# Optimization experiments

Measured on AMD Instinct MI355X. Metric: run time of the kernel, lower is better.

Reference implementation:

```python
import jax, jax.numpy as jnp
import numpy as np

L = 3          # num_layer
E_DIM = 64     # emb_dim
B = 4          # graphs per batch
N = 20000      # nodes per graph
E = 320000     # edges per graph
IN_DIM = 21    # raw node feature dim (Linear(21, emb_dim))
BN_EPS = 1e-5


def setup_inputs() -> dict:
    key = jax.random.key(0)
    ks = jax.random.split(key, 16)
    h2 = 2 * E_DIM
    inp = {
        "x": jax.random.normal(ks[0], (B, N, IN_DIM), dtype=jnp.float32),
        "edge_index": jax.random.randint(ks[1], (B, 2, E), 0, N, dtype=jnp.int64),
        "edge_attr": jax.random.normal(ks[2], (B, E, 1), dtype=jnp.float32),
        # layer-0 input node embedding Linear(21, emb)
        "inW": jax.random.normal(ks[3], (IN_DIM, E_DIM), dtype=jnp.float32) * 0.1,
        "inb": jnp.zeros((E_DIM,), dtype=jnp.float32),
        # per-layer edge encoder Linear(1, emb)
        "edgeW": jax.random.normal(ks[4], (L, 1, E_DIM), dtype=jnp.float32) * 0.1,
        "edgeb": jnp.zeros((L, E_DIM), dtype=jnp.float32),
        # per-layer MLP: Linear(2e,2e) -> BN(2e) -> ReLU -> Linear(2e,e)
        "W1": jax.random.normal(ks[5], (L, h2, h2), dtype=jnp.float32) * 0.05,
        "b1": jnp.zeros((L, h2), dtype=jnp.float32),
        "gamma": jnp.ones((L, h2), dtype=jnp.float32),
        "beta": jnp.zeros((L, h2), dtype=jnp.float32),
        "W2": jax.random.normal(ks[6], (L, h2, E_DIM), dtype=jnp.float32) * 0.05,
        "b2": jnp.zeros((L, E_DIM), dtype=jnp.float32),
    }
    return inp


def _batchnorm_train(h, g, b):
    # BatchNorm1d in training mode: per-graph stats over the node dim, biased var
    m = h.mean(axis=0)
    v = jnp.mean((h - m) ** 2, axis=0)
    return (h - m) * jax.lax.rsqrt(v + BN_EPS) * g + b


def _gin_layer(xg, eig, eag, W1l, b1l, gl, bel, W2l, b2l):
    # xg [N,e], eig [2,E], eag [E,e]
    x_j = xg[eig[0]]                                   # gather source nodes [E,e]
    msg = jnp.concatenate([x_j, eag], axis=-1)         # [E,2e]
    aggr = jax.ops.segment_sum(msg, eig[1], num_segments=N)  # scatter-add [N,2e]
    h = aggr @ W1l + b1l
    h = _batchnorm_train(h, gl, bel)
    h = jax.nn.relu(h)
    return h @ W2l + b2l                               # [N,e]


def reference(x, edge_index, edge_attr, inW, inb, edgeW, edgeb, W1, b1, gamma, beta, W2, b2):
    h = x
    for l in range(L):
        ea = edge_attr @ edgeW[l] + edgeb[l]           # [B,E,e] edge embeddings
        if l == 0:
            h = h @ inW + inb                          # [B,N,e]
        h = jax.vmap(_gin_layer, in_axes=(0, 0, 0, None, None, None, None, None, None))(
            h, edge_index, ea, W1[l], b1[l], gamma[l], beta[l], W2[l], b2[l])
        if l < L - 1:                                  # drop_ratio=0 -> dropout is identity
            h = jax.nn.relu(h)
    return h  # JK='last'
```

## Files before the change

### kernel.cpp

```cpp
#include <hip/hip_runtime.h>
#include <hip/hip_bf16.h>
#include <hip/hip_fp16.h>

#define NB 4
#define NN 20000
#define NE 320000
#define IND 21
#define ED 64
#define H2 128
#define CAP 48
#define NRANGE 32
#define RNODES 625
#define BINCAP 160
#define SCAP 11264
#define BN_EPS 1e-5f

typedef __attribute__((ext_vector_type(8))) short bf16x8;
typedef __attribute__((ext_vector_type(4))) float f32x4;

__device__ __forceinline__ short f2bf(float f) {
    unsigned u = __float_as_uint(f);
    u += 0x7fffu + ((u >> 16) & 1u);
    return (short)(u >> 16);
}

__device__ __forceinline__ void add8(float* ac, const uint4 rv) {
    const float2 f0 = __half22float2(*(const __half2*)&rv.x);
    const float2 f1 = __half22float2(*(const __half2*)&rv.y);
    const float2 f2 = __half22float2(*(const __half2*)&rv.z);
    const float2 f3 = __half22float2(*(const __half2*)&rv.w);
    ac[0] += f0.x; ac[1] += f0.y; ac[2] += f1.x; ac[3] += f1.y;
    ac[4] += f2.x; ac[5] += f2.y; ac[6] += f3.x; ac[7] += f3.y;
}


__global__ __launch_bounds__(256) void k_compact(
    const int* __restrict__ ei, const float* __restrict__ eattr,
    uint2* __restrict__ stage, int* __restrict__ rcnt)
{
    __shared__ uint2 bins[NRANGE][BINCAP];
    __shared__ int lcnt[NRANGE];
    __shared__ int lbase[NRANGE];
    const int b = blockIdx.y;
    const int e0 = blockIdx.x * 2048;
    const int tid = threadIdx.x;
    if (tid < NRANGE) lcnt[tid] = 0;
    __syncthreads();
    const int* srcp = ei + (size_t)b * 2 * NE;
    const int* dstp = srcp + NE;
    const float* ap = eattr + (size_t)b * NE;
    #pragma unroll
    for (int it = 0; it < 8; ++it) {
        const int e = e0 + it * 256 + tid;
        if (e < NE) {
            const int dst = dstp[e];
            const int src = srcp[e];
            const float a = ap[e];
            const int r = dst / RNODES;
            const unsigned lo = ((unsigned)src & 0xffffu) | (__float_as_uint(a) & 0xffff0000u);
            const int p = atomicAdd(&lcnt[r], 1);
            if (p < BINCAP) bins[r][p] = make_uint2(lo, (unsigned)dst);
        }
    }
    __syncthreads();
    if (tid < NRANGE) lbase[tid] = atomicAdd(&rcnt[b * NRANGE + tid], min(lcnt[tid], BINCAP));
    __syncthreads();
    for (int r = 0; r < NRANGE; ++r) {
        const int c = min(lcnt[r], BINCAP);
        uint2* dstg = stage + (size_t)(b * NRANGE + r) * SCAP + lbase[r];
        for (int i = tid; i < c; i += 256) dstg[i] = bins[r][i];
    }
}

__global__ __launch_bounds__(256) void k_scatter(
    const uint2* __restrict__ stage, const int* __restrict__ rcnt,
    int* __restrict__ cnt, unsigned int* __restrict__ bucket)
{
    const int b = blockIdx.x >> 5;
    const int g = blockIdx.x & 31;
    const int count = min(rcnt[b * NRANGE + g], SCAP);
    const uint2* st = stage + (size_t)(b * NRANGE + g) * SCAP;
    for (int idx = threadIdx.x; idx < count; idx += 256) {
        const uint2 rec = st[idx];
        const int node = b * NN + (int)rec.y;
        const int p = atomicAdd(&cnt[node], 1);
        if (p < CAP) bucket[(size_t)node * CAP + p] = rec.x;
    }
}

__global__ __launch_bounds__(256) void k_in(
    const float* __restrict__ x, const float* __restrict__ inW,
    const float* __restrict__ inb, __half* __restrict__ h)
{
    const int b = blockIdx.y;
    const int t = blockIdx.x * 256 + threadIdx.x;
    const int n = t >> 6;
    const int c = t & 63;
    if (n >= NN) return;
    const float* xr = x + ((size_t)b * NN + n) * IND;
    float acc = inb[c];
    #pragma unroll
    for (int k = 0; k < IND; ++k) acc += xr[k] * inW[k * ED + c];
    h[((size_t)b * NN + n) * ED + c] = __float2half(acc);
}

__global__ __launch_bounds__(256) void k_prep(
    const float* __restrict__ W1, const float* __restrict__ W2,
    const float* __restrict__ edgeW, const float* __restrict__ edgeb,
    short* __restrict__ W1T, short* __restrict__ W2T,
    float* __restrict__ uv_all, float* __restrict__ stats_all)
{
    const int l = blockIdx.x;
    const int tid = threadIdx.x;
    ((float4*)(stats_all + l * 1024))[tid] = make_float4(0.f, 0.f, 0.f, 0.f);
    for (int i = tid; i < H2 * ED; i += 256) {
        const int j = i >> 6, k = i & 63;
        W1T[l * 8192 + i] = f2bf(W1[(size_t)l * H2 * H2 + k * H2 + j]);
    }
    for (int i = tid; i < ED * H2; i += 256) {
        const int c = i >> 7, k = i & 127;
        W2T[l * 8192 + i] = f2bf(W2[(size_t)l * H2 * ED + k * ED + c]);
    }
    if (tid < H2) {
        float u = 0.f, v = 0.f;
        for (int k = 0; k < ED; ++k) {
            const float w = W1[(size_t)l * H2 * H2 + (ED + k) * H2 + tid];
            u += edgeW[l * ED + k] * w;
            v += edgeb[l * ED + k] * w;
        }
        uv_all[l * 256 + tid] = u;
        uv_all[l * 256 + H2 + tid] = v;
    }
}


__global__ __launch_bounds__(256, 4) void k_aggr_stats(
    const __half* __restrict__ h, const unsigned int* __restrict__ bucket,
    const int* __restrict__ cnt_arr, const short* __restrict__ W1Tl,
    const float* __restrict__ b1l, const float* __restrict__ uv_l,
    short* __restrict__ aggr_bf, float* __restrict__ s_attr,
    float* __restrict__ stats_l, int write_sattr)
{
    __shared__ short atb[32 * 72];
    __shared__ float sdl[32], ddl[32];
    __shared__ float uL[H2], vL[H2], bbL[H2];
    const int tid = threadIdx.x;
    const int g = blockIdx.x & 7;
    const int b = g >> 1;
    const int t = ((int)blockIdx.x >> 3) * 2 + (g & 1);
    if (t >= NN / 32) return;
    const int n0 = t * 32;

    if (tid < H2) { uL[tid] = uv_l[tid]; vL[tid] = uv_l[H2 + tid]; bbL[tid] = b1l[tid]; }

    {
        const int node = n0 + (tid >> 3);
        const int q = tid & 7;
        const int cntraw = cnt_arr[b * NN + node];
        const int cnt = min(cntraw, CAP);
        const unsigned int* row = bucket + (size_t)(b * NN + node) * CAP;
        const __half* hp = h + (size_t)b * NN * ED + q * 8;
        float ac[8];
        #pragma unroll
        for (int i = 0; i < 8; ++i) ac[i] = 0.f;
        float sa = 0.f;
        int j = 0;
        for (; j + 8 <= cnt; j += 8) {
            const uint4 sA = *(const uint4*)(row + j);
            const uint4 sB = *(const uint4*)(row + j + 4);
            const uint4 r0 = *(const uint4*)(hp + (size_t)(sA.x & 0xffffu) * ED);
            const uint4 r1 = *(const uint4*)(hp + (size_t)(sA.y & 0xffffu) * ED);
            const uint4 r2 = *(const uint4*)(hp + (size_t)(sA.z & 0xffffu) * ED);
            const uint4 r3 = *(const uint4*)(hp + (size_t)(sA.w & 0xffffu) * ED);
            const uint4 r4 = *(const uint4*)(hp + (size_t)(sB.x & 0xffffu) * ED);
            const uint4 r5 = *(const uint4*)(hp + (size_t)(sB.y & 0xffffu) * ED);
            const uint4 r6 = *(const uint4*)(hp + (size_t)(sB.z & 0xffffu) * ED);
            const uint4 r7 = *(const uint4*)(hp + (size_t)(sB.w & 0xffffu) * ED);
            sa += __uint_as_float(sA.x & 0xffff0000u) + __uint_as_float(sA.y & 0xffff0000u)
                + __uint_as_float(sA.z & 0xffff0000u) + __uint_as_float(sA.w & 0xffff0000u)
                + __uint_as_float(sB.x & 0xffff0000u) + __uint_as_float(sB.y & 0xffff0000u)
                + __uint_as_float(sB.z & 0xffff0000u) + __uint_as_float(sB.w & 0xffff0000u);
            add8(ac, r0); add8(ac, r1); add8(ac, r2); add8(ac, r3);
            add8(ac, r4); add8(ac, r5); add8(ac, r6); add8(ac, r7);
        }
        for (; j + 4 <= cnt; j += 4) {
            const uint4 ss = *(const uint4*)(row + j);
            const uint4 r0 = *(const uint4*)(hp + (size_t)(ss.x & 0xffffu) * ED);
            const uint4 r1 = *(const uint4*)(hp + (size_t)(ss.y & 0xffffu) * ED);
            const uint4 r2 = *(const uint4*)(hp + (size_t)(ss.z & 0xffffu) * ED);
            const uint4 r3 = *(const uint4*)(hp + (size_t)(ss.w & 0xffffu) * ED);
            sa += __uint_as_float(ss.x & 0xffff0000u) + __uint_as_float(ss.y & 0xffff0000u)
                + __uint_as_float(ss.z & 0xffff0000u) + __uint_as_float(ss.w & 0xffff0000u);
            add8(ac, r0); add8(ac, r1); add8(ac, r2); add8(ac, r3);
        }
        for (; j < cnt; ++j) {
            const unsigned e = row[j];
            sa += __uint_as_float(e & 0xffff0000u);
            const uint4 r0 = *(const uint4*)(hp + (size_t)(e & 0xffffu) * ED);
            add8(ac, r0);
        }
        uint4 pk;
        pk.x = (unsigned short)f2bf(ac[0]) | ((unsigned int)(unsigned short)f2bf(ac[1]) << 16);
        pk.y = (unsigned short)f2bf(ac[2]) | ((unsigned int)(unsigned short)f2bf(ac[3]) << 16);
        pk.z = (unsigned short)f2bf(ac[4]) | ((unsigned int)(unsigned short)f2bf(ac[5]) << 16);
        pk.w = (unsigned short)f2bf(ac[6]) | ((unsigned int)(unsigned short)f2bf(ac[7]) << 16);
        *(uint4*)&atb[(tid >> 3) * 72 + q * 8] = pk;
        *(uint4*)&aggr_bf[((size_t)b * NN + node) * ED + q * 8] = pk;
        if (q == 0) {
            sdl[tid >> 3] = sa;
            ddl[tid >> 3] = (float)cntraw;
            if (write_sattr) s_attr[b * NN + node] = sa;
        }
    }
    __syncthreads();

    const int l = tid & 63;
    const int w = tid >> 6;
    const int m = l & 15, quad = l >> 4;
    const int mt = w & 1;
    const int jb = (w >> 1) * 4;
    f32x4 acc[4];
    #pragma unroll
    for (int i = 0; i < 4; ++i) acc[i] = (f32x4){0.f, 0.f, 0.f, 0.f};
    #pragma unroll
    for (int kc = 0; kc < 2; ++kc) {
        const bf16x8 fa = *(const bf16x8*)&atb[(mt * 16 + m) * 72 + kc * 32 + quad * 8];
        #pragma unroll
        for (int t2 = 0; t2 < 4; ++t2) {
            const bf16x8 fb = *(const bf16x8*)&W1Tl[((jb + t2) * 16 + m) * 64 + kc * 32 + quad * 8];
            acc[t2] = __builtin_amdgcn_mfma_f32_16x16x32_bf16(fa, fb, acc[t2], 0, 0, 0);
        }
    }
    float sa_r[4], dg_r[4];
    #pragma unroll
    for (int r = 0; r < 4; ++r) {
        const int row = mt * 16 + quad * 4 + r;
        sa_r[r] = sdl[row]; dg_r[r] = ddl[row];
    }
    #pragma unroll
    for (int t2 = 0; t2 < 4; ++t2) {
        const int j = (jb + t2) * 16 + m;
        const float u = uL[j], v = vL[j], bb = bbL[j];
        float ls = 0.f, lq = 0.f;
        #pragma unroll
        for (int r = 0; r < 4; ++r) {
            const float h1 = acc[t2][r] + sa_r[r] * u + dg_r[r] * v + bb;
            ls += h1; lq += h1 * h1;
        }
        ls += __shfl_xor(ls, 16); ls += __shfl_xor(ls, 32);
        lq += __shfl_xor(lq, 16); lq += __shfl_xor(lq, 32);
        if (l < 16) {
            atomicAdd(&stats_l[b * H2 + j], ls);
            atomicAdd(&stats_l[NB * H2 + b * H2 + j], lq);
        }
    }
}

__global__ __launch_bounds__(256) void k_mlp_out(
    const short* __restrict__ aggr_bf, const float* __restrict__ s_attr,
    const int* __restrict__ cnt_arr, const short* __restrict__ W1Tl,
    const short* __restrict__ W2Tl, const float* __restrict__ b1l,
    const float* __restrict__ uv_l, const float* __restrict__ stats_l,
    const float* __restrict__ gamma_l, const float* __restrict__ beta_l,
    const float* __restrict__ b2l, __half* __restrict__ outh,
    float* __restrict__ outf, int last)
{
    __shared__ short wt[H2 * 72];
    __shared__ short ab[64 * 72];
    __shared__ short pb[64 * 136];
    __shared__ float sdl[64], ddl[64];
    __shared__ float uL[H2], vL[H2], bbL[H2], scL[H2], shL[H2];
    const int tid = threadIdx.x;
    const int g = blockIdx.x & 7;
    const int b = g >> 1;
    const int t = ((int)blockIdx.x >> 3) * 2 + (g & 1);
    if (t >= (NN + 63) / 64) return;
    const int n0 = t * 64;

    for (int i = tid; i < 1024; i += 256)
        *(uint4*)&wt[(i >> 3) * 72 + (i & 7) * 8] = ((const uint4*)W1Tl)[i];
    for (int i = tid; i < 512; i += 256)
        *(uint4*)&ab[(i >> 3) * 72 + (i & 7) * 8] =
            ((const uint4*)(aggr_bf + ((size_t)b * NN + n0) * ED))[i];
    if (tid < 64) sdl[tid] = s_attr[b * NN + n0 + tid];
    else if (tid < 128) ddl[tid - 64] = (float)cnt_arr[b * NN + n0 + tid - 64];
    if (tid < H2) {
        const int j = tid;
        const float mm = stats_l[b * H2 + j] * (1.f / NN);
        const float var = fmaxf(stats_l[NB * H2 + b * H2 + j] * (1.f / NN) - mm * mm, 0.f);
        const float rs = rsqrtf(var + BN_EPS);
        const float sc = gamma_l[j] * rs;
        scL[j] = sc;
        shL[j] = beta_l[j] - mm * sc;
        uL[j] = uv_l[j]; vL[j] = uv_l[H2 + j]; bbL[j] = b1l[j];
    }
    __syncthreads();

    const int l = tid & 63;
    const int w = tid >> 6;
    const int m = l & 15, quad = l >> 4;
    {
        f32x4 acc[8];
        #pragma unroll
        for (int i = 0; i < 8; ++i) acc[i] = (f32x4){0.f, 0.f, 0.f, 0.f};
        #pragma unroll
        for (int kc = 0; kc < 2; ++kc) {
            const bf16x8 fa = *(const bf16x8*)&ab[(w * 16 + m) * 72 + kc * 32 + quad * 8];
            #pragma unroll
            for (int t2 = 0; t2 < 8; ++t2) {
                const bf16x8 fb = *(const bf16x8*)&wt[(t2 * 16 + m) * 72 + kc * 32 + quad * 8];
                acc[t2] = __builtin_amdgcn_mfma_f32_16x16x32_bf16(fa, fb, acc[t2], 0, 0, 0);
            }
        }
        float sa_r[4], dg_r[4];
        #pragma unroll
        for (int r = 0; r < 4; ++r) {
            const int row = w * 16 + quad * 4 + r;
            sa_r[r] = sdl[row]; dg_r[r] = ddl[row];
        }
        #pragma unroll
        for (int t2 = 0; t2 < 8; ++t2) {
            const int j = t2 * 16 + m;
            const float u = uL[j], v = vL[j], bb = bbL[j];
            const float sc = scL[j], sh = shL[j];
            #pragma unroll
            for (int r = 0; r < 4; ++r) {
                const float h1 = acc[t2][r] + sa_r[r] * u + dg_r[r] * v + bb;
                pb[(w * 16 + quad * 4 + r) * 136 + j] = f2bf(fmaxf(h1 * sc + sh, 0.f));
            }
        }
    }
    __syncthreads();
    for (int i = tid; i < 1024; i += 256)
        *(uint4*)&wt[(i >> 4) * 136 + (i & 15) * 8] = ((const uint4*)W2Tl)[i];
    __syncthreads();
    {
        f32x4 acc2[4];
        #pragma unroll
        for (int i = 0; i < 4; ++i) acc2[i] = (f32x4){0.f, 0.f, 0.f, 0.f};
        #pragma unroll
        for (int kc = 0; kc < 4; ++kc) {
            const bf16x8 fa = *(const bf16x8*)&pb[(w * 16 + m) * 136 + kc * 32 + quad * 8];
            #pragma unroll
            for (int t2 = 0; t2 < 4; ++t2) {
                const bf16x8 fb = *(const bf16x8*)&wt[(t2 * 16 + m) * 136 + kc * 32 + quad * 8];
                acc2[t2] = __builtin_amdgcn_mfma_f32_16x16x32_bf16(fa, fb, acc2[t2], 0, 0, 0);
            }
        }
        #pragma unroll
        for (int t2 = 0; t2 < 4; ++t2) {
            const int c = t2 * 16 + m;
            const float bb2 = b2l[c];
            #pragma unroll
            for (int r = 0; r < 4; ++r) {
                const int row = w * 16 + quad * 4 + r;
                const int n = n0 + row;
                if (n < NN) {
                    const size_t idx = ((size_t)b * NN + n) * ED + c;
                    float o = acc2[t2][r] + bb2;
                    if (last) outf[idx] = o;
                    else outh[idx] = __float2half(fmaxf(o, 0.f));
                }
            }
        }
    }
}


extern "C" void kernel_launch(void* const* d_in, const int* in_sizes, int n_in,
                              void* d_out, int out_size, void* d_ws, size_t ws_size,
                              hipStream_t stream) {
    const float* x     = (const float*)d_in[0];
    const int*   ei    = (const int*)d_in[1];
    const float* eattr = (const float*)d_in[2];
    const float* inW   = (const float*)d_in[3];
    const float* inb   = (const float*)d_in[4];
    const float* edgeW = (const float*)d_in[5];
    const float* edgeb = (const float*)d_in[6];
    const float* W1    = (const float*)d_in[7];
    const float* b1    = (const float*)d_in[8];
    const float* gamma = (const float*)d_in[9];
    const float* beta  = (const float*)d_in[10];
    const float* W2    = (const float*)d_in[11];
    const float* b2    = (const float*)d_in[12];
    float* out = (float*)d_out;

    float* s_attr = (float*)d_ws;
    int*   cnt    = (int*)(s_attr + NB * NN);
    int*   rcnt   = cnt + NB * NN;
    uint2* stage  = (uint2*)(rcnt + 128);
    unsigned int* bucket = (unsigned int*)(stage + (size_t)NB * NRANGE * SCAP);
    short* aggr_bf = (short*)(bucket + (size_t)NB * NN * CAP);
    __half* hh    = (__half*)(aggr_bf + (size_t)NB * NN * ED);
    short* W1T    = (short*)(hh + (size_t)NB * NN * ED);
    short* W2T    = W1T + 3 * 8192;
    float* uv_all = (float*)(W2T + 3 * 8192);
    float* stats  = uv_all + 3 * 256;

    hipMemsetAsync(cnt, 0, ((size_t)NB * NN + 128) * sizeof(int), stream);

    k_compact<<<dim3((NE + 2047) / 2048, NB), 256, 0, stream>>>(ei, eattr, stage, rcnt);
    k_scatter<<<NB * NRANGE, 256, 0, stream>>>(stage, rcnt, cnt, bucket);
    k_in<<<dim3(NN * ED / 256, NB), 256, 0, stream>>>(x, inW, inb, hh);
    k_prep<<<3, 256, 0, stream>>>(W1, W2, edgeW, edgeb, W1T, W2T, uv_all, stats);

    const int nblk1 = 8 * ((NN / 32 + 1) / 2);
    const int nblk2 = 8 * (((NN + 63) / 64 + 1) / 2);
    for (int l = 0; l < 3; ++l) {
        k_aggr_stats<<<nblk1, 256, 0, stream>>>(hh, bucket, cnt,
            W1T + l * 8192, b1 + l * H2, uv_all + l * 256,
            aggr_bf, s_attr, stats + l * 1024, (l == 0) ? 1 : 0);
        k_mlp_out<<<nblk2, 256, 0, stream>>>(aggr_bf, s_attr, cnt,
            W1T + l * 8192, W2T + l * 8192, b1 + l * H2, uv_all + l * 256,
            stats + l * 1024, gamma + l * H2, beta + l * H2, b2 + l * ED,
            hh, out, (l == 2) ? 1 : 0);
    }
}
```

Before: 368.4 us.

## Materialize pre-BN hidden activations instead of recomputing first GEMM in output kernel

The aggregation kernel now writes the pre-BatchNorm hidden activation h1 (128 channels, fp16) to global memory. It no longer writes the bf16 aggregate and the per-node attribute sums. The output kernel reads h1 directly, applies the BN scale and shift with ReLU in registers, and runs only the second GEMM, so the W1 MFMA pass, the W1 shared-memory staging and one barrier disappear. In exchange, the intermediate per node doubles in size (128 fp16 versus 64 bf16), and h1 is stored with narrow per-lane 2-byte writes, which raises global memory traffic.

```diff
diff --git a/kernel.cpp b/kernel.cpp
--- a/kernel.cpp
+++ b/kernel.cpp
@@ -138,8 +138,7 @@
     const __half* __restrict__ h, const unsigned int* __restrict__ bucket,
     const int* __restrict__ cnt_arr, const short* __restrict__ W1Tl,
     const float* __restrict__ b1l, const float* __restrict__ uv_l,
-    short* __restrict__ aggr_bf, float* __restrict__ s_attr,
-    float* __restrict__ stats_l, int write_sattr)
+    __half* __restrict__ h1g, float* __restrict__ stats_l)
 {
     __shared__ short atb[32 * 72];
     __shared__ float sdl[32], ddl[32];
@@ -205,11 +204,9 @@
         pk.z = (unsigned short)f2bf(ac[4]) | ((unsigned int)(unsigned short)f2bf(ac[5]) << 16);
         pk.w = (unsigned short)f2bf(ac[6]) | ((unsigned int)(unsigned short)f2bf(ac[7]) << 16);
         *(uint4*)&atb[(tid >> 3) * 72 + q * 8] = pk;
-        *(uint4*)&aggr_bf[((size_t)b * NN + node) * ED + q * 8] = pk;
         if (q == 0) {
             sdl[tid >> 3] = sa;
             ddl[tid >> 3] = (float)cntraw;
-            if (write_sattr) s_attr[b * NN + node] = sa;
         }
     }
     __syncthreads();
@@ -244,8 +241,9 @@
         float ls = 0.f, lq = 0.f;
         #pragma unroll
         for (int r = 0; r < 4; ++r) {
-            const float h1 = acc[t2][r] + sa_r[r] * u + dg_r[r] * v + bb;
-            ls += h1; lq += h1 * h1;
+            const float h1v = acc[t2][r] + sa_r[r] * u + dg_r[r] * v + bb;
+            h1g[((size_t)b * NN + n0 + mt * 16 + quad * 4 + r) * H2 + j] = __float2half(h1v);
+            ls += h1v; lq += h1v * h1v;
         }
         ls += __shfl_xor(ls, 16); ls += __shfl_xor(ls, 32);
         lq += __shfl_xor(lq, 16); lq += __shfl_xor(lq, 32);
@@ -257,19 +255,13 @@
 }
 
 __global__ __launch_bounds__(256) void k_mlp_out(
-    const short* __restrict__ aggr_bf, const float* __restrict__ s_attr,
-    const int* __restrict__ cnt_arr, const short* __restrict__ W1Tl,
-    const short* __restrict__ W2Tl, const float* __restrict__ b1l,
-    const float* __restrict__ uv_l, const float* __restrict__ stats_l,
-    const float* __restrict__ gamma_l, const float* __restrict__ beta_l,
-    const float* __restrict__ b2l, __half* __restrict__ outh,
-    float* __restrict__ outf, int last)
-{
-    __shared__ short wt[H2 * 72];
-    __shared__ short ab[64 * 72];
+    const __half* __restrict__ h1g, const short* __restrict__ W2Tl,
+    const float* __restrict__ stats_l, const float* __restrict__ gamma_l,
+    const float* __restrict__ beta_l, const float* __restrict__ b2l,
+    __half* __restrict__ outh, float* __restrict__ outf, int last)
+{
+    __shared__ short wt[ED * 136];
     __shared__ short pb[64 * 136];
-    __shared__ float sdl[64], ddl[64];
-    __shared__ float uL[H2], vL[H2], bbL[H2], scL[H2], shL[H2];
     const int tid = threadIdx.x;
     const int g = blockIdx.x & 7;
     const int b = g >> 1;
@@ -277,64 +269,50 @@
     if (t >= (NN + 63) / 64) return;
     const int n0 = t * 64;
 
+    const uint4* h1p = (const uint4*)(h1g + ((size_t)b * NN + n0) * H2);
+    const uint4 hv0 = h1p[tid];
+    const uint4 hv1 = h1p[tid + 256];
+    const uint4 hv2 = h1p[tid + 512];
+    const uint4 hv3 = h1p[tid + 768];
+
     for (int i = tid; i < 1024; i += 256)
-        *(uint4*)&wt[(i >> 3) * 72 + (i & 7) * 8] = ((const uint4*)W1Tl)[i];
-    for (int i = tid; i < 512; i += 256)
-        *(uint4*)&ab[(i >> 3) * 72 + (i & 7) * 8] =
-            ((const uint4*)(aggr_bf + ((size_t)b * NN + n0) * ED))[i];
-    if (tid < 64) sdl[tid] = s_attr[b * NN + n0 + tid];
-    else if (tid < 128) ddl[tid - 64] = (float)cnt_arr[b * NN + n0 + tid - 64];
-    if (tid < H2) {
-        const int j = tid;
+        *(uint4*)&wt[(i >> 4) * 136 + (i & 15) * 8] = ((const uint4*)W2Tl)[i];
+
+    const int ch0 = (tid & 15) * 8;
+    float sc[8], sh[8];
+    #pragma unroll
+    for (int e = 0; e < 8; ++e) {
+        const int j = ch0 + e;
         const float mm = stats_l[b * H2 + j] * (1.f / NN);
         const float var = fmaxf(stats_l[NB * H2 + b * H2 + j] * (1.f / NN) - mm * mm, 0.f);
         const float rs = rsqrtf(var + BN_EPS);
-        const float sc = gamma_l[j] * rs;
-        scL[j] = sc;
-        shL[j] = beta_l[j] - mm * sc;
-        uL[j] = uv_l[j]; vL[j] = uv_l[H2 + j]; bbL[j] = b1l[j];
-    }
-    __syncthreads();
-
-    const int l = tid & 63;
-    const int w = tid >> 6;
-    const int m = l & 15, quad = l >> 4;
+        sc[e] = gamma_l[j] * rs;
+        sh[e] = beta_l[j] - mm * sc[e];
+    }
+
     {
-        f32x4 acc[8];
-        #pragma unroll
-        for (int i = 0; i < 8; ++i) acc[i] = (f32x4){0.f, 0.f, 0.f, 0.f};
-        #pragma unroll
-        for (int kc = 0; kc < 2; ++kc) {
-            const bf16x8 fa = *(const bf16x8*)&ab[(w * 16 + m) * 72 + kc * 32 + quad * 8];
-            #pragma unroll
-            for (int t2 = 0; t2 < 8; ++t2) {
-                const bf16x8 fb = *(const bf16x8*)&wt[(t2 * 16 + m) * 72 + kc * 32 + quad * 8];
-                acc[t2] = __builtin_amdgcn_mfma_f32_16x16x32_bf16(fa, fb, acc[t2], 0, 0, 0);
-            }
-        }
-        float sa_r[4], dg_r[4];
-        #pragma unroll
-        for (int r = 0; r < 4; ++r) {
-            const int row = w * 16 + quad * 4 + r;
-            sa_r[r] = sdl[row]; dg_r[r] = ddl[row];
-        }
-        #pragma unroll
-        for (int t2 = 0; t2 < 8; ++t2) {
-            const int j = t2 * 16 + m;
-            const float u = uL[j], v = vL[j], bb = bbL[j];
-            const float sc = scL[j], sh = shL[j];
-            #pragma unroll
-            for (int r = 0; r < 4; ++r) {
-                const float h1 = acc[t2][r] + sa_r[r] * u + dg_r[r] * v + bb;
-                pb[(w * 16 + quad * 4 + r) * 136 + j] = f2bf(fmaxf(h1 * sc + sh, 0.f));
-            }
-        }
-    }
-    __syncthreads();
-    for (int i = tid; i < 1024; i += 256)
-        *(uint4*)&wt[(i >> 4) * 136 + (i & 15) * 8] = ((const uint4*)W2Tl)[i];
-    __syncthreads();
+        uint4 hv;
+        short ob[8];
+        #define BN8(K, HV)                                                    \
+        {                                                                     \
+            hv = HV;                                                          \
+            const __half* hp = (const __half*)&hv;                            \
+            _Pragma("unroll")                                                 \
+            for (int e = 0; e < 8; ++e) {                                     \
+                const float xv = __half2float(hp[e]);                         \
+                ob[e] = f2bf(fmaxf(xv * sc[e] + sh[e], 0.f));                 \
+            }                                                                 \
+            *(uint4*)&pb[((tid >> 4) + (K) * 16) * 136 + ch0] = *(uint4*)ob;  \
+        }
+        BN8(0, hv0) BN8(1, hv1) BN8(2, hv2) BN8(3, hv3)
+        #undef BN8
+    }
+    __syncthreads();
+
     {
+        const int l = tid & 63;
+        const int w = tid >> 6;
+        const int m = l & 15, quad = l >> 4;
         f32x4 acc2[4];
         #pragma unroll
         for (int i = 0; i < 4; ++i) acc2[i] = (f32x4){0.f, 0.f, 0.f, 0.f};
@@ -385,14 +363,13 @@
     const float* b2    = (const float*)d_in[12];
     float* out = (float*)d_out;
 
-    float* s_attr = (float*)d_ws;
-    int*   cnt    = (int*)(s_attr + NB * NN);
+    int*   cnt    = (int*)d_ws;
     int*   rcnt   = cnt + NB * NN;
     uint2* stage  = (uint2*)(rcnt + 128);
     unsigned int* bucket = (unsigned int*)(stage + (size_t)NB * NRANGE * SCAP);
-    short* aggr_bf = (short*)(bucket + (size_t)NB * NN * CAP);
-    __half* hh    = (__half*)(aggr_bf + (size_t)NB * NN * ED);
-    short* W1T    = (short*)(hh + (size_t)NB * NN * ED);
+    __half* hh    = (__half*)(bucket + (size_t)NB * NN * CAP);
+    __half* h1g   = hh + (size_t)NB * NN * ED;
+    short* W1T    = (short*)(h1g + (size_t)NB * NN * H2);
     short* W2T    = W1T + 3 * 8192;
     float* uv_all = (float*)(W2T + 3 * 8192);
     float* stats  = uv_all + 3 * 256;
@@ -409,10 +386,10 @@
     for (int l = 0; l < 3; ++l) {
         k_aggr_stats<<<nblk1, 256, 0, stream>>>(hh, bucket, cnt,
             W1T + l * 8192, b1 + l * H2, uv_all + l * 256,
-            aggr_bf, s_attr, stats + l * 1024, (l == 0) ? 1 : 0);
-        k_mlp_out<<<nblk2, 256, 0, stream>>>(aggr_bf, s_attr, cnt,
-            W1T + l * 8192, W2T + l * 8192, b1 + l * H2, uv_all + l * 256,
-            stats + l * 1024, gamma + l * H2, beta + l * H2, b2 + l * ED,
+            h1g, stats + l * 1024);
+        k_mlp_out<<<nblk2, 256, 0, stream>>>(h1g,
+            W2T + l * 8192, stats + l * 1024,
+            gamma + l * H2, beta + l * H2, b2 + l * ED,
             hh, out, (l == 2) ? 1 : 0);
     }
 }
```

After: 360.7 us. -2.1%, faster.
